# Kernel optimization log

Measured on AMD Instinct MI355X. Metric: run time of the kernel, lower is better.

The kernel has to match this reference:

```python
import jax, jax.numpy as jnp
import numpy as np

H, K, D = 24, 2, 128          # query heads, kv heads, head_size
HIDDEN = H * D                # 3072
ROPE_THETA = 10000.0


def setup_inputs() -> dict:
    key = jax.random.key(0)
    ks = jax.random.split(key, 6)
    B, S = 2, 2048
    T = B * S
    hidden_states = jax.random.normal(ks[0], (T, HIDDEN), dtype=jnp.float32)
    w_qkv = jax.random.normal(ks[1], ((H + 2 * K) * D, HIDDEN), dtype=jnp.float32) * (HIDDEN ** -0.5)
    b_qkv = jax.random.normal(ks[2], ((H + 2 * K) * D,), dtype=jnp.float32) * 0.02
    w_o = jax.random.normal(ks[3], (HIDDEN, H * D), dtype=jnp.float32) * (HIDDEN ** -0.5)
    b_o = jax.random.normal(ks[4], (HIDDEN,), dtype=jnp.float32) * 0.02
    # rotary tables: positions restart per sequence (flash-varlen prefill layout)
    pos = jnp.tile(jnp.arange(S, dtype=jnp.float32), B)            # [T]
    inv_freq = 1.0 / (ROPE_THETA ** (jnp.arange(0, D, 2, dtype=jnp.float32) / D))  # [D/2]
    freqs = pos[:, None] * inv_freq[None, :]                        # [T, D/2]
    return {
        "hidden_states": hidden_states,
        "w_qkv": w_qkv, "b_qkv": b_qkv,
        "w_o": w_o, "b_o": b_o,
        "cos": jnp.cos(freqs), "sin": jnp.sin(freqs),
        "seq_len": S, "window": 1024,
    }


def _rope(x, cos, sin):
    # rotate-half (neox) style, as in TGI PositionRotaryEmbedding
    half = x.shape[-1] // 2
    x1, x2 = x[..., :half], x[..., half:]
    c, s = cos[:, None, :], sin[:, None, :]   # broadcast over head dim
    return jnp.concatenate([x1 * c - x2 * s, x2 * c + x1 * s], axis=-1)


def reference(hidden_states, w_qkv, b_qkv, w_o, b_o, cos, sin, seq_len, window):
    T = hidden_states.shape[0]
    B = T // seq_len
    scale = D ** -0.5

    # fused QKV projection
    qkv = hidden_states @ w_qkv.T + b_qkv                 # [T, (H+2K)*D]
    q = qkv[:, : H * D].reshape(T, H, D)
    kv = qkv[:, H * D:].reshape(T, 2, K, D)
    k, v = kv[:, 0], kv[:, 1]                             # [T, K, D]

    q = _rope(q, cos, sin)
    k = _rope(k, cos, sin)

    # GQA: expand kv heads to query heads
    groups = H // K
    qb = q.reshape(B, seq_len, H, D)
    kb = jnp.repeat(k.reshape(B, seq_len, K, D), groups, axis=2)  # [B,S,H,D]
    vb = jnp.repeat(v.reshape(B, seq_len, K, D), groups, axis=2)

    scores = jnp.einsum("bqhd,bkhd->bhqk", qb, kb) * scale        # [B,H,S,S]
    idx = jnp.arange(seq_len)
    delta = idx[:, None] - idx[None, :]
    mask = (delta >= 0) & (delta < window)                        # causal + sliding window
    scores = jnp.where(mask[None, None], scores, jnp.float32(-1e9))
    attn = jax.nn.softmax(scores, axis=-1)
    out = jnp.einsum("bhqk,bkhd->bqhd", attn, vb).reshape(T, H * D)
    return out @ w_o.T + b_o
```

## Files before the change

kernel.cpp:

```cpp
#include <hip/hip_runtime.h>
#include <hip/hip_bf16.h>

typedef __attribute__((ext_vector_type(8))) short bf16x8;
typedef __attribute__((ext_vector_type(4))) float f32x4;

__device__ __forceinline__ short f2bf_bits(float f) {
    __hip_bfloat16 h = __float2bfloat16(f);
    short s;
    __builtin_memcpy(&s, &h, 2);
    return s;
}

__device__ __forceinline__ float bf_bits2f(short s) {
    unsigned int u = ((unsigned int)(unsigned short)s) << 16;
    float f;
    __builtin_memcpy(&f, &u, 4);
    return f;
}

__device__ __forceinline__ bf16x8 load8(const float* p) {
    float4 a = *(const float4*)p;
    float4 b = *(const float4*)(p + 4);
    bf16x8 r;
    r[0] = f2bf_bits(a.x); r[1] = f2bf_bits(a.y);
    r[2] = f2bf_bits(a.z); r[3] = f2bf_bits(a.w);
    r[4] = f2bf_bits(b.x); r[5] = f2bf_bits(b.y);
    r[6] = f2bf_bits(b.z); r[7] = f2bf_bits(b.w);
    return r;
}
__device__ __forceinline__ bf16x8 load8(const __hip_bfloat16* p) {
    return *(const bf16x8*)p;
}

__device__ __forceinline__ void store_out(__hip_bfloat16* p, float v) {
    *p = __float2bfloat16(v);
}
__device__ __forceinline__ void store_out(float* p, float v) { *p = v; }

__device__ __forceinline__ void stage16(const __hip_bfloat16* g, short* lds_base, int lane) {
#if defined(__has_builtin) && __has_builtin(__builtin_amdgcn_global_load_lds)
    __builtin_amdgcn_global_load_lds(
        (__attribute__((address_space(1))) void*)g,
        (__attribute__((address_space(3))) void*)lds_base, 16, 0, 0);
#else
    *(bf16x8*)(lds_base + lane * 8) = *(const bf16x8*)g;
#endif
}

__global__ void cvt3_f32_bf16(const float* __restrict__ a, short* __restrict__ da, int na8,
                              const float* __restrict__ b, short* __restrict__ db, int nb8,
                              const float* __restrict__ c, short* __restrict__ dc, int nc8) {
    int i = blockIdx.x * 256 + threadIdx.x;
    if (i < na8) {
        *(bf16x8*)(da + (size_t)i * 8) = load8(a + (size_t)i * 8);
    } else if ((i -= na8) < nb8) {
        *(bf16x8*)(db + (size_t)i * 8) = load8(b + (size_t)i * 8);
    } else if ((i -= nb8) < nc8) {
        *(bf16x8*)(dc + (size_t)i * 8) = load8(c + (size_t)i * 8);
    }
}

template <typename TC>
__global__ __launch_bounds__(256) void gemm_bt_lds(
    const __hip_bfloat16* __restrict__ A, const __hip_bfloat16* __restrict__ B,
    const float* __restrict__ bias, TC* __restrict__ C, int M, int N, int K)
{
    __shared__ short As[128 * 32];
    __shared__ short Bs[128 * 32];

    const int tid  = threadIdx.x;
    const int lane = tid & 63;
    const int wid  = tid >> 6;
    const int quad = lane >> 4;
    const int m16  = lane & 15;

    const int nT = gridDim.x;
    int lin = blockIdx.y * nT + blockIdx.x;
    int grp = lin >> 3;
    int bm8 = lin & 7;
    int bn  = grp % nT;
    int bm  = (grp / nT) * 8 + bm8;

    const int mBase = bm * 128;
    const int nBase = bn * 128;
    const int wm = (wid >> 1) * 64;
    const int wn = (wid & 1) * 64;

    f32x4 acc[4][4] = {};

    const int lrow = lane >> 2;
    const int lcol = (lane & 3) * 8;
    const __hip_bfloat16* Abase = A + (size_t)(mBase + wid * 32 + lrow) * K + lcol;
    const __hip_bfloat16* Bbase = B + (size_t)(nBase + wid * 32 + lrow) * K + lcol;
    short* AsW = &As[wid * 32 * 32];
    short* BsW = &Bs[wid * 32 * 32];

    for (int kt = 0; kt < K; kt += 32) {
        __syncthreads();
        stage16(Abase + kt,          AsW,           lane);
        stage16(Abase + 16 * K + kt, AsW + 16 * 32, lane);
        stage16(Bbase + kt,          BsW,           lane);
        stage16(Bbase + 16 * K + kt, BsW + 16 * 32, lane);
        __syncthreads();

        bf16x8 afr[4], bfr[4];
        #pragma unroll
        for (int i = 0; i < 4; ++i)
            afr[i] = *(const bf16x8*)(&As[(wm + 16 * i + m16) * 32 + quad * 8]);
        #pragma unroll
        for (int j = 0; j < 4; ++j)
            bfr[j] = *(const bf16x8*)(&Bs[(wn + 16 * j + m16) * 32 + quad * 8]);
        #pragma unroll
        for (int i = 0; i < 4; ++i)
            #pragma unroll
            for (int j = 0; j < 4; ++j)
                acc[i][j] = __builtin_amdgcn_mfma_f32_16x16x32_bf16(
                    afr[i], bfr[j], acc[i][j], 0, 0, 0);
    }

    float bv[4];
    #pragma unroll
    for (int j = 0; j < 4; ++j)
        bv[j] = bias[nBase + wn + 16 * j + m16];

    #pragma unroll
    for (int i = 0; i < 4; ++i)
        #pragma unroll
        for (int j = 0; j < 4; ++j) {
            int col = nBase + wn + 16 * j + m16;
            #pragma unroll
            for (int r = 0; r < 4; ++r) {
                int row = mBase + wm + 16 * i + quad * 4 + r;
                store_out(&C[(size_t)row * N + col], acc[i][j][r] + bv[j]);
            }
        }
}

#define LDSS 40

template <typename TA, typename TB, typename TC>
__global__ __launch_bounds__(256) void gemm_bt_bias(
    const TA* __restrict__ A, const TB* __restrict__ B,
    const float* __restrict__ bias, TC* __restrict__ C, int M, int N, int K)
{
    __shared__ short As[128 * LDSS];
    __shared__ short Bs[128 * LDSS];

    const int tid  = threadIdx.x;
    const int lane = tid & 63;
    const int wid  = tid >> 6;
    const int quad = lane >> 4;
    const int m16  = lane & 15;

    const int mBase = blockIdx.y * 128;
    const int nBase = blockIdx.x * 128;
    const int wm = (wid >> 1) * 64;
    const int wn = (wid & 1) * 64;

    f32x4 acc[4][4] = {};
    const int srow = tid >> 2;
    const int sgrp = (tid & 3) * 8;

    for (int kt = 0; kt < K; kt += 32) {
        __syncthreads();
        for (int p = 0; p < 2; ++p) {
            int r = srow + p * 64;
            *(bf16x8*)(&As[r * LDSS + sgrp]) =
                load8(A + (size_t)(mBase + r) * K + kt + sgrp);
            *(bf16x8*)(&Bs[r * LDSS + sgrp]) =
                load8(B + (size_t)(nBase + r) * K + kt + sgrp);
        }
        __syncthreads();

        bf16x8 afr[4], bfr[4];
        #pragma unroll
        for (int i = 0; i < 4; ++i)
            afr[i] = *(const bf16x8*)(&As[(wm + 16 * i + m16) * LDSS + quad * 8]);
        #pragma unroll
        for (int j = 0; j < 4; ++j)
            bfr[j] = *(const bf16x8*)(&Bs[(wn + 16 * j + m16) * LDSS + quad * 8]);
        #pragma unroll
        for (int i = 0; i < 4; ++i)
            #pragma unroll
            for (int j = 0; j < 4; ++j)
                acc[i][j] = __builtin_amdgcn_mfma_f32_16x16x32_bf16(
                    afr[i], bfr[j], acc[i][j], 0, 0, 0);
    }

    float bv[4];
    #pragma unroll
    for (int j = 0; j < 4; ++j)
        bv[j] = bias[nBase + wn + 16 * j + m16];

    #pragma unroll
    for (int i = 0; i < 4; ++i)
        #pragma unroll
        for (int j = 0; j < 4; ++j) {
            int col = nBase + wn + 16 * j + m16;
            #pragma unroll
            for (int r = 0; r < 4; ++r) {
                int row = mBase + wm + 16 * i + quad * 4 + r;
                store_out(&C[(size_t)row * N + col], acc[i][j][r] + bv[j]);
            }
        }
}

__global__ void rope_kernel(__hip_bfloat16* __restrict__ qkv,
                            const float* __restrict__ cosb,
                            const float* __restrict__ sinb, int T)
{
    int idx = blockIdx.x * 256 + threadIdx.x;
    int total = T * 26 * 8;
    if (idx >= total) return;
    int j = idx & 7;
    int h = (idx >> 3) % 26;
    int t = idx / (26 * 8);
    int col = (h < 24) ? h * 128 : 3072 + (h - 24) * 128;
    int d0 = j * 8;
    size_t base = (size_t)t * 3584 + col + d0;
    bf16x8 x1 = *(const bf16x8*)((const short*)qkv + base);
    bf16x8 x2 = *(const bf16x8*)((const short*)qkv + base + 64);
    float4 c0 = *(const float4*)(cosb + t * 64 + d0);
    float4 c1 = *(const float4*)(cosb + t * 64 + d0 + 4);
    float4 s0 = *(const float4*)(sinb + t * 64 + d0);
    float4 s1 = *(const float4*)(sinb + t * 64 + d0 + 4);
    float cc[8] = {c0.x, c0.y, c0.z, c0.w, c1.x, c1.y, c1.z, c1.w};
    float ss[8] = {s0.x, s0.y, s0.z, s0.w, s1.x, s1.y, s1.z, s1.w};
    bf16x8 o1, o2;
    #pragma unroll
    for (int i = 0; i < 8; ++i) {
        float f1 = bf_bits2f(x1[i]);
        float f2 = bf_bits2f(x2[i]);
        o1[i] = f2bf_bits(f1 * cc[i] - f2 * ss[i]);
        o2[i] = f2bf_bits(f2 * cc[i] + f1 * ss[i]);
    }
    *(bf16x8*)((short*)qkv + base)      = o1;
    *(bf16x8*)((short*)qkv + base + 64) = o2;
}

#define SM_SHIFT 12.0f

__global__ __launch_bounds__(256, 3) void attn_kernel(
    const __hip_bfloat16* __restrict__ qkv,
    __hip_bfloat16* __restrict__ out,
    const int* __restrict__ seq_len_p, const int* __restrict__ window_p)
{
    const int S = seq_len_p[0];
    const int window = window_p[0];
    const float scale = 0.088388347648318447f;

    const int h   = blockIdx.y;
    const int kvh = h / 12;
    const int tid  = threadIdx.x;
    const int lane = tid & 63;
    const int wid  = tid >> 6;
    const int quad = lane >> 4;
    const int m16  = lane & 15;

    const int qb_global = blockIdx.x * 128;
    const int b  = qb_global / S;
    const int qb = qb_global - b * S;

    __shared__ short Vt[128 * 72];
    __shared__ short Ps[4][32 * 40];

    const size_t kvrow0 = (size_t)(b * S) * 3584 + 3072 + kvh * 128;

    bf16x8 qf[2][4];
    {
        const __hip_bfloat16* qp =
            qkv + (size_t)(qb_global + wid * 32 + m16) * 3584 + h * 128;
        #pragma unroll
        for (int qt = 0; qt < 2; ++qt)
            #pragma unroll
            for (int dc = 0; dc < 4; ++dc)
                qf[qt][dc] = *(const bf16x8*)(qp + qt * 16 * 3584 + dc * 32 + quad * 8);
    }

    f32x4 accO[2][8] = {};
    float lqt[2] = {0.f, 0.f};

    int ka0 = qb - window + 1;
    if (ka0 < 0) ka0 = 0;
    ka0 &= ~31;
    const int kend = qb + 128;

    for (int kt = ka0; kt < kend; kt += 32) {
        __syncthreads();
        #pragma unroll
        for (int p = 0; p < 2; ++p) {
            int L   = tid + p * 256;
            int key = L & 31;
            int gg  = L >> 5;
            int d0  = gg * 8;
            bf16x8 v8 = *(const bf16x8*)(qkv + kvrow0 + (size_t)(kt + key) * 3584 + 256 + d0);
            short* dst = &Vt[d0 * 72 + key + (gg & 1) * 32];
            #pragma unroll
            for (int i2 = 0; i2 < 8; ++i2) dst[i2 * 72] = v8[i2];
        }
        __syncthreads();

        f32x4 sacc[2][2] = {};
        #pragma unroll
        for (int st = 0; st < 2; ++st) {
            const __hip_bfloat16* kp =
                qkv + kvrow0 + (size_t)(kt + st * 16 + m16) * 3584;
            #pragma unroll
            for (int dc = 0; dc < 4; ++dc) {
                bf16x8 kf = *(const bf16x8*)(kp + dc * 32 + quad * 8);
                sacc[st][0] = __builtin_amdgcn_mfma_f32_16x16x32_bf16(
                    kf, qf[0][dc], sacc[st][0], 0, 0, 0);
                sacc[st][1] = __builtin_amdgcn_mfma_f32_16x16x32_bf16(
                    kf, qf[1][dc], sacc[st][1], 0, 0, 0);
            }
        }

        #pragma unroll
        for (int qt = 0; qt < 2; ++qt) {
            const int qmin = qb + wid * 32 + qt * 16;
            short* prow = &Ps[wid][(qt * 16 + m16) * 40];
            float psum = 0.f;
            if (kt <= qmin - 31 && kt >= qmin + 16 - window) {
                #pragma unroll
                for (int st = 0; st < 2; ++st)
                    #pragma unroll
                    for (int r = 0; r < 4; ++r) {
                        float pp = __expf(fminf(
                            sacc[st][qt][r] * scale - SM_SHIFT, 80.f));
                        psum += pp;
                        prow[st * 16 + quad * 4 + r] = f2bf_bits(pp);
                    }
            } else {
                const int dl_base = (qmin + m16) - (kt + quad * 4);
                #pragma unroll
                for (int st = 0; st < 2; ++st)
                    #pragma unroll
                    for (int r = 0; r < 4; ++r) {
                        int dl = dl_base - st * 16 - r;
                        float pp = ((unsigned)dl < (unsigned)window)
                            ? __expf(fminf(sacc[st][qt][r] * scale - SM_SHIFT, 80.f))
                            : 0.f;
                        psum += pp;
                        prow[st * 16 + quad * 4 + r] = f2bf_bits(pp);
                    }
            }
            psum += __shfl_xor(psum, 16, 64);
            psum += __shfl_xor(psum, 32, 64);
            lqt[qt] += psum;
        }

        bf16x8 pf0 = *(const bf16x8*)(&Ps[wid][(0  + m16) * 40 + quad * 8]);
        bf16x8 pf1 = *(const bf16x8*)(&Ps[wid][(16 + m16) * 40 + quad * 8]);
        #pragma unroll
        for (int dt = 0; dt < 8; ++dt) {
            int row = dt * 16 + m16;
            bf16x8 vf = *(const bf16x8*)(&Vt[row * 72 + quad * 8 + ((row >> 3) & 1) * 32]);
            accO[0][dt] = __builtin_amdgcn_mfma_f32_16x16x32_bf16(pf0, vf, accO[0][dt], 0, 0, 0);
            accO[1][dt] = __builtin_amdgcn_mfma_f32_16x16x32_bf16(pf1, vf, accO[1][dt], 0, 0, 0);
        }
    }

    #pragma unroll
    for (int qt = 0; qt < 2; ++qt) {
        float li[4];
        #pragma unroll
        for (int r = 0; r < 4; ++r)
            li[r] = 1.0f / __shfl(lqt[qt], quad * 4 + r, 64);
        #pragma unroll
        for (int r = 0; r < 4; ++r) {
            int t = qb_global + wid * 32 + qt * 16 + quad * 4 + r;
            __hip_bfloat16* op = out + (size_t)t * 3072 + h * 128 + m16;
            #pragma unroll
            for (int dt = 0; dt < 8; ++dt)
                op[dt * 16] = __float2bfloat16(accO[qt][dt][r] * li[r]);
        }
    }
}

extern "C" void kernel_launch(void* const* d_in, const int* in_sizes, int n_in,
                              void* d_out, int out_size, void* d_ws, size_t ws_size,
                              hipStream_t stream) {
    const float* hidden = (const float*)d_in[0];
    const float* w_qkv  = (const float*)d_in[1];
    const float* b_qkv  = (const float*)d_in[2];
    const float* w_o    = (const float*)d_in[3];
    const float* b_o    = (const float*)d_in[4];
    const float* cosb   = (const float*)d_in[5];
    const float* sinb   = (const float*)d_in[6];
    const int* seq_len_p = (const int*)d_in[7];
    const int* window_p  = (const int*)d_in[8];

    const int HID  = in_sizes[4];
    const int NQKV = in_sizes[2];
    const int T    = in_sizes[0] / HID;

    size_t off = 0;
    auto alloc = [&](size_t bytes) {
        char* p = (char*)d_ws + off;
        off = (off + bytes + 255) & ~(size_t)255;
        return p;
    };
    __hip_bfloat16* qkv      = (__hip_bfloat16*)alloc((size_t)T * NQKV * 2);
    __hip_bfloat16* attn_out = (__hip_bfloat16*)alloc((size_t)T * HID * 2);
    __hip_bfloat16* hid_bf = (__hip_bfloat16*)alloc((size_t)T * HID * 2);
    __hip_bfloat16* wq_bf  = (__hip_bfloat16*)alloc((size_t)NQKV * HID * 2);
    __hip_bfloat16* wo_bf  = (__hip_bfloat16*)alloc((size_t)HID * HID * 2);
    const bool pre = (ws_size >= off);

    dim3 blk(256);

    if (pre) {
        int n8h = T * HID / 8, n8q = NQKV * HID / 8, n8o = HID * HID / 8;
        int n8 = n8h + n8q + n8o;
        cvt3_f32_bf16<<<dim3((n8 + 255) / 256), blk, 0, stream>>>(
            hidden, (short*)hid_bf, n8h, w_qkv, (short*)wq_bf, n8q,
            w_o, (short*)wo_bf, n8o);
        gemm_bt_lds<__hip_bfloat16><<<dim3(NQKV / 128, T / 128), blk, 0, stream>>>(
            hid_bf, wq_bf, b_qkv, qkv, T, NQKV, HID);
    } else {
        gemm_bt_bias<float, float, __hip_bfloat16>
            <<<dim3(NQKV / 128, T / 128), blk, 0, stream>>>(
            hidden, w_qkv, b_qkv, qkv, T, NQKV, HID);
    }

    int total = T * 26 * 8;
    rope_kernel<<<dim3((total + 255) / 256), blk, 0, stream>>>(qkv, cosb, sinb, T);

    attn_kernel<<<dim3(T / 128, 24), blk, 0, stream>>>(qkv, attn_out, seq_len_p, window_p);

    if (pre) {
        gemm_bt_lds<float><<<dim3(HID / 128, T / 128), blk, 0, stream>>>(
            attn_out, wo_bf, b_o, (float*)d_out, T, HID, HID);
    } else {
        gemm_bt_bias<__hip_bfloat16, float, float>
            <<<dim3(HID / 128, T / 128), blk, 0, stream>>>(
            attn_out, w_o, b_o, (float*)d_out, T, HID, HID);
    }
}
```

Measured before the change: 572.7 us.

## Replace 128x128 GEMM with 256x256 double-buffered 8-wave pipelined kernel

Replaces the 128x128 tile bf16 GEMM used for the QKV and output projections with a 256x256 tile, 512-thread kernel. It double-buffers 128KB of LDS with XOR-swizzled direct global-to-LDS loads and interleaves staging with MFMA phases, using explicit waitcnt, barriers and setprio. Blocks are remapped across the grid to improve L2 locality. The aim is more data reuse per tile and overlap of global loads with compute, at the cost of fewer workgroups (QKV grid 14x16, output 12x16) and heavy LDS use that limits occupancy to one block per CU.

New measurement: 479.5 us. 1.19x faster.

```diff
diff --git a/kernel.cpp b/kernel.cpp
--- a/kernel.cpp
+++ b/kernel.cpp
@@ -36,16 +36,6 @@
     *p = __float2bfloat16(v);
 }
 __device__ __forceinline__ void store_out(float* p, float v) { *p = v; }
-
-__device__ __forceinline__ void stage16(const __hip_bfloat16* g, short* lds_base, int lane) {
-#if defined(__has_builtin) && __has_builtin(__builtin_amdgcn_global_load_lds)
-    __builtin_amdgcn_global_load_lds(
-        (__attribute__((address_space(1))) void*)g,
-        (__attribute__((address_space(3))) void*)lds_base, 16, 0, 0);
-#else
-    *(bf16x8*)(lds_base + lane * 8) = *(const bf16x8*)g;
-#endif
-}
 
 __global__ void cvt3_f32_bf16(const float* __restrict__ a, short* __restrict__ da, int na8,
                               const float* __restrict__ b, short* __restrict__ db, int nb8,
@@ -60,80 +50,181 @@
     }
 }
 
+#define GB_REG 65536
+
+__device__ __forceinline__ int half_off(int buf, int half) {
+    return buf * 32768 + half * 16384;
+}
+
 template <typename TC>
-__global__ __launch_bounds__(256) void gemm_bt_lds(
+__global__ __launch_bounds__(512) void gemm256(
     const __hip_bfloat16* __restrict__ A, const __hip_bfloat16* __restrict__ B,
     const float* __restrict__ bias, TC* __restrict__ C, int M, int N, int K)
 {
-    __shared__ short As[128 * 32];
-    __shared__ short Bs[128 * 32];
+    __shared__ char smem[131072];
 
     const int tid  = threadIdx.x;
     const int lane = tid & 63;
     const int wid  = tid >> 6;
     const int quad = lane >> 4;
     const int m16  = lane & 15;
-
-    const int nT = gridDim.x;
-    int lin = blockIdx.y * nT + blockIdx.x;
-    int grp = lin >> 3;
-    int bm8 = lin & 7;
-    int bn  = grp % nT;
-    int bm  = (grp / nT) * 8 + bm8;
-
-    const int mBase = bm * 128;
-    const int nBase = bn * 128;
-    const int wm = (wid >> 1) * 64;
-    const int wn = (wid & 1) * 64;
-
-    f32x4 acc[4][4] = {};
-
-    const int lrow = lane >> 2;
-    const int lcol = (lane & 3) * 8;
-    const __hip_bfloat16* Abase = A + (size_t)(mBase + wid * 32 + lrow) * K + lcol;
-    const __hip_bfloat16* Bbase = B + (size_t)(nBase + wid * 32 + lrow) * K + lcol;
-    short* AsW = &As[wid * 32 * 32];
-    short* BsW = &Bs[wid * 32 * 32];
-
-    for (int kt = 0; kt < K; kt += 32) {
-        __syncthreads();
-        stage16(Abase + kt,          AsW,           lane);
-        stage16(Abase + 16 * K + kt, AsW + 16 * 32, lane);
-        stage16(Bbase + kt,          BsW,           lane);
-        stage16(Bbase + 16 * K + kt, BsW + 16 * 32, lane);
-        __syncthreads();
-
-        bf16x8 afr[4], bfr[4];
-        #pragma unroll
-        for (int i = 0; i < 4; ++i)
-            afr[i] = *(const bf16x8*)(&As[(wm + 16 * i + m16) * 32 + quad * 8]);
-        #pragma unroll
-        for (int j = 0; j < 4; ++j)
-            bfr[j] = *(const bf16x8*)(&Bs[(wn + 16 * j + m16) * 32 + quad * 8]);
-        #pragma unroll
-        for (int i = 0; i < 4; ++i)
-            #pragma unroll
-            for (int j = 0; j < 4; ++j)
-                acc[i][j] = __builtin_amdgcn_mfma_f32_16x16x32_bf16(
-                    afr[i], bfr[j], acc[i][j], 0, 0, 0);
-    }
+    const int wmg  = wid >> 2;
+    const int wng  = wid & 3;
+    const int bhalf = wng >> 1;
+    const int bsub  = (wng & 1) * 4;
+
+    const int gx  = gridDim.x;
+    const int nwg = gx * gridDim.y;
+    int lin = blockIdx.y * gx + blockIdx.x;
+    if ((nwg & 7) == 0) {
+        int q = nwg >> 3;
+        lin = (lin & 7) * q + (lin >> 3);
+    }
+    const int bn = lin % gx, bm = lin / gx;
+    const int mBase = bm * 256, nBase = bn * 256;
+
+    const int roff = (m16 << 6) | ((quad * 16) ^ ((m16 & 8) << 2));
+
+    int r_s[2], c_s[2];
+    #pragma unroll
+    for (int l = 0; l < 2; ++l) {
+        int sub = l * 8 + wid;
+        int r16 = (tid >> 2) & 15;
+        int cb  = ((tid & 3) * 16) ^ ((r16 & 8) << 2);
+        r_s[l] = (sub >> 1) * 16 + r16;
+        c_s[l] = (sub & 1) * 32 + (cb >> 1);
+    }
+
+    const __hip_bfloat16* Ab = A + (size_t)mBase * K;
+    const __hip_bfloat16* Bb = B + (size_t)nBase * K;
+
+    auto stage = [&](int region, const __hip_bfloat16* base, int buf, int half, int tile) {
+        const __hip_bfloat16* gb = base + (size_t)(half * 128) * K + tile * 64;
+        #pragma unroll
+        for (int l = 0; l < 2; ++l) {
+            const __hip_bfloat16* g = gb + (size_t)r_s[l] * K + c_s[l];
+            short* lb = (short*)(smem + region + half_off(buf, half) + l * 8192 + wid * 1024);
+            __builtin_amdgcn_global_load_lds(
+                (__attribute__((address_space(1))) void*)g,
+                (__attribute__((address_space(3))) void*)lb, 16, 0, 0);
+        }
+    };
+
+    f32x4 acc[8][4] = {};
+    bf16x8 afr[4][2];
+    bf16x8 bfr[2][2][2];
+
+    auto LD_A = [&](int buf, int g) {
+        const char* base = smem + half_off(buf, wmg) + (g ? 8192 : 0);
+        #pragma unroll
+        for (int m = 0; m < 4; ++m)
+            #pragma unroll
+            for (int ks = 0; ks < 2; ++ks)
+                afr[m][ks] = *(const bf16x8*)(base + ((m * 2 + ks) << 10) + roff);
+    };
+    auto LD_B = [&](int buf, int g) {
+        const char* base = smem + GB_REG + half_off(buf, bhalf) + ((bsub + g * 2) << 11);
+        #pragma unroll
+        for (int j = 0; j < 2; ++j)
+            #pragma unroll
+            for (int ks = 0; ks < 2; ++ks)
+                bfr[g][j][ks] = *(const bf16x8*)(base + ((j * 2 + ks) << 10) + roff);
+    };
+    auto MM = [&](int mo, int g) {
+        #pragma unroll
+        for (int m = 0; m < 4; ++m)
+            #pragma unroll
+            for (int j = 0; j < 2; ++j)
+                #pragma unroll
+                for (int ks = 0; ks < 2; ++ks)
+                    acc[mo + m][g * 2 + j] = __builtin_amdgcn_mfma_f32_16x16x32_bf16(
+                        afr[m][ks], bfr[g][j][ks], acc[mo + m][g * 2 + j], 0, 0, 0);
+    };
+
+#define SBAR() __builtin_amdgcn_s_barrier()
+#define WAIT_LGKM0() do { asm volatile("s_waitcnt lgkmcnt(0)" ::: "memory"); \
+                          __builtin_amdgcn_sched_barrier(0); } while (0)
+#define WAIT_VM4()   do { asm volatile("s_waitcnt vmcnt(4)"   ::: "memory"); \
+                          __builtin_amdgcn_sched_barrier(0); } while (0)
+
+    const int NT = K >> 6;
+
+    stage(GB_REG, Bb, 0, 0, 0);
+    stage(0,      Ab, 0, 0, 0);
+    stage(GB_REG, Bb, 0, 1, 0);
+    stage(0,      Ab, 0, 1, 0);
+    stage(GB_REG, Bb, 1, 0, 1);
+    stage(0,      Ab, 1, 0, 1);
+    WAIT_VM4();
+    SBAR();
+
+    for (int i = 0; i < (NT >> 1); ++i) {
+        const int to = 2 * i + 1;
+        const int t2 = min(2 * i + 2, NT - 1);
+        const int t3 = min(2 * i + 3, NT - 1);
+        LD_A(0, 0); LD_B(0, 0);
+        stage(GB_REG, Bb, 1, 1, to);
+        SBAR(); WAIT_LGKM0();
+        __builtin_amdgcn_s_setprio(1); MM(0, 0); __builtin_amdgcn_s_setprio(0);
+        SBAR();
+        LD_B(0, 1);
+        stage(0, Ab, 1, 1, to);
+        SBAR(); WAIT_LGKM0();
+        __builtin_amdgcn_s_setprio(1); MM(0, 1); __builtin_amdgcn_s_setprio(0);
+        SBAR();
+        LD_A(0, 1);
+        stage(GB_REG, Bb, 0, 0, t2);
+        SBAR(); WAIT_LGKM0();
+        __builtin_amdgcn_s_setprio(1); MM(4, 1); __builtin_amdgcn_s_setprio(0);
+        SBAR();
+        stage(0, Ab, 0, 0, t2);
+        WAIT_VM4();
+        SBAR();
+        __builtin_amdgcn_s_setprio(1); MM(4, 0); __builtin_amdgcn_s_setprio(0);
+        SBAR();
+        LD_A(1, 0); LD_B(1, 0);
+        stage(GB_REG, Bb, 0, 1, t2);
+        SBAR(); WAIT_LGKM0();
+        __builtin_amdgcn_s_setprio(1); MM(0, 0); __builtin_amdgcn_s_setprio(0);
+        SBAR();
+        LD_B(1, 1);
+        stage(0, Ab, 0, 1, t2);
+        SBAR(); WAIT_LGKM0();
+        __builtin_amdgcn_s_setprio(1); MM(0, 1); __builtin_amdgcn_s_setprio(0);
+        SBAR();
+        LD_A(1, 1);
+        stage(GB_REG, Bb, 1, 0, t3);
+        SBAR(); WAIT_LGKM0();
+        __builtin_amdgcn_s_setprio(1); MM(4, 1); __builtin_amdgcn_s_setprio(0);
+        SBAR();
+        stage(0, Ab, 1, 0, t3);
+        WAIT_VM4();
+        SBAR();
+        __builtin_amdgcn_s_setprio(1); MM(4, 0); __builtin_amdgcn_s_setprio(0);
+        SBAR();
+    }
+
+#undef SBAR
+#undef WAIT_LGKM0
+#undef WAIT_VM4
 
     float bv[4];
     #pragma unroll
     for (int j = 0; j < 4; ++j)
-        bv[j] = bias[nBase + wn + 16 * j + m16];
-
-    #pragma unroll
-    for (int i = 0; i < 4; ++i)
+        bv[j] = bias[nBase + wng * 64 + j * 16 + m16];
+
+    #pragma unroll
+    for (int mf = 0; mf < 8; ++mf) {
         #pragma unroll
         for (int j = 0; j < 4; ++j) {
-            int col = nBase + wn + 16 * j + m16;
+            const int col = nBase + wng * 64 + j * 16 + m16;
             #pragma unroll
             for (int r = 0; r < 4; ++r) {
-                int row = mBase + wm + 16 * i + quad * 4 + r;
-                store_out(&C[(size_t)row * N + col], acc[i][j][r] + bv[j]);
+                const int row = mBase + wmg * 128 + mf * 16 + quad * 4 + r;
+                store_out(&C[(size_t)row * N + col], acc[mf][j][r] + bv[j]);
             }
         }
+    }
 }
 
 #define LDSS 40
@@ -406,16 +497,18 @@
     __hip_bfloat16* wq_bf  = (__hip_bfloat16*)alloc((size_t)NQKV * HID * 2);
     __hip_bfloat16* wo_bf  = (__hip_bfloat16*)alloc((size_t)HID * HID * 2);
     const bool pre = (ws_size >= off);
+    const bool big = pre && (T % 256 == 0) && (NQKV % 256 == 0) &&
+                     (HID % 256 == 0) && (HID % 64 == 0);
 
     dim3 blk(256);
 
-    if (pre) {
+    if (big) {
         int n8h = T * HID / 8, n8q = NQKV * HID / 8, n8o = HID * HID / 8;
         int n8 = n8h + n8q + n8o;
         cvt3_f32_bf16<<<dim3((n8 + 255) / 256), blk, 0, stream>>>(
             hidden, (short*)hid_bf, n8h, w_qkv, (short*)wq_bf, n8q,
             w_o, (short*)wo_bf, n8o);
-        gemm_bt_lds<__hip_bfloat16><<<dim3(NQKV / 128, T / 128), blk, 0, stream>>>(
+        gemm256<__hip_bfloat16><<<dim3(NQKV / 256, T / 256), dim3(512), 0, stream>>>(
             hid_bf, wq_bf, b_qkv, qkv, T, NQKV, HID);
     } else {
         gemm_bt_bias<float, float, __hip_bfloat16>
@@ -428,8 +521,8 @@
 
     attn_kernel<<<dim3(T / 128, 24), blk, 0, stream>>>(qkv, attn_out, seq_len_p, window_p);
 
-    if (pre) {
-        gemm_bt_lds<float><<<dim3(HID / 128, T / 128), blk, 0, stream>>>(
+    if (big) {
+        gemm256<float><<<dim3(HID / 256, T / 256), dim3(512), 0, stream>>>(
             attn_out, wo_bf, b_o, (float*)d_out, T, HID, HID);
     } else {
         gemm_bt_bias<__hip_bfloat16, float, float>
```
